# Kernel tuning notes

Hardware: AMD Instinct MI355X
Metric: run time of the kernel (lower is better)

Reference implementation:

```python
import jax, jax.numpy as jnp
import numpy as np

B, I, J, DIN, DOUT = 256, 1152, 10, 8, 16
ROUTING_ITERS = 3


def squash(v):
    # v: [..., D]; squash(v) = (|v|^2 / (1+|v|^2)) * v/|v| = v * |v| / (1+|v|^2)
    l2 = jnp.linalg.norm(v, axis=-1, keepdims=True)
    return v * (l2 / (1.0 + l2 * l2))


def setup_inputs() -> dict:
    key = jax.random.key(0)
    k1, k2 = jax.random.split(key)
    x = jax.random.normal(k1, (B, I, DIN), dtype=jnp.float32)
    # per-(i,j) Linear(DIN -> DOUT, bias=False) weights, stacked: [I, J, DOUT, DIN]
    W = jax.random.normal(k2, (I, J, DOUT, DIN), dtype=jnp.float32) * 0.1
    return {"x": x, "W": W}


def reference(x, W):
    # prediction vectors u[b,i,j,:] = W[i,j] @ x[b,i,:]  -> [B, I, J, DOUT]
    u = jnp.einsum('bid,ijod->bijo', x, W)
    b = jnp.zeros((I, J), dtype=u.dtype)  # routing logits (shared across batch)
    s = None
    for _ in range(ROUTING_ITERS):
        c = jax.nn.softmax(b, axis=-1)              # [I, J]
        s = jnp.einsum('ij,bijd->bjd', c, u)        # coupling-weighted sum over in-caps
        s = squash(s)                               # [B, J, DOUT]
        # agreement: b[i,j] += sum_b <u[b,i,j], s[b,j]>
        b = b + jnp.einsum('bijd,bjd->ij', u, s)
    return s
```

## Files before the change

### kernel.cpp

```cpp
#include <hip/hip_runtime.h>
#include <math.h>

typedef unsigned short ushort_t;
typedef __attribute__((ext_vector_type(8))) __bf16 bf16x8;
typedef __attribute__((ext_vector_type(4))) float floatx4;

#define B_    256
#define I_    1152
#define J_    10
#define DIN_  8
#define DOUT_ 16
#define K_    (I_*DIN_)
#define N_    (J_*DOUT_)
#define KSPLIT 16
#define KCHUNK (K_/KSPLIT)
#define KSTEPS (KCHUNK/32)

#define CHUNK16 2368

static __device__ __forceinline__ ushort_t f2bf(float f) {
    unsigned int u = __float_as_uint(f);
    u += 0x7fffu + ((u >> 16) & 1u);
    return (ushort_t)(u >> 16);
}
static __device__ __forceinline__ float bf2f(ushort_t h) {
    return __uint_as_float(((unsigned int)h) << 16);
}

__global__ __launch_bounds__(256)
void prep_xpack_kernel(const float* __restrict__ x, ushort_t* __restrict__ xPk)
{
    const int gid = blockIdx.x * 256 + threadIdx.x;
    const int f   = gid * 8;
    const int row = f / K_;
    const int kk  = f - row * K_;
    const int kc  = kk / KCHUNK;
    const int t   = kk - kc * KCHUNK;
    const int s   = t >> 5;
    const int q   = (t & 31) >> 3;
    const int mb  = row >> 4, r = row & 15;

    const float* src = x + (size_t)f;
    bf16x8 h8, l8;
    #pragma unroll
    for (int e = 0; e < 8; ++e) {
        float v = src[e];
        __bf16 h = (__bf16)v;
        h8[e] = h;
        l8[e] = (__bf16)(v - (float)h);
    }
    bf16x8* dst = (bf16x8*)xPk + (size_t)(mb * 16 + kc) * CHUNK16 + s * 128 + q * 16 + r;
    dst[0]  = h8;
    dst[64] = l8;
}

__global__ __launch_bounds__(256)
void prep_wpack_kernel(const float* __restrict__ W, float* __restrict__ wPk)
{
    const int gid = blockIdx.x * 256 + threadIdx.x;
    const int f   = gid * 4;
    const int i   = f / 1280;
    const int rem = f - i * 1280;
    const int no  = rem >> 3;
    const int p   = (rem >> 2) & 1;
    const int nt  = no >> 4, r = no & 15;
    const int kc  = i / 72;
    const int m   = i - kc * 72;
    const int s   = m >> 2, q = m & 3;

    float4 v = *(const float4*)(W + (size_t)f);
    ((float4*)wPk)[(size_t)(nt * 16 + kc) * CHUNK16 + (s * 2 + p) * 64 + q * 16 + r] = v;
}

__global__ __launch_bounds__(128)
void gemm_s_part_kernel(const ushort_t* __restrict__ xPk, const float* __restrict__ wPk,
                        const float* __restrict__ blog,
                        float* __restrict__ pbuf, const int iter)
{
    const int tid  = threadIdx.x;
    const int blk  = blockIdx.x;
    const int kb   = blk & 7;
    const int tile = blk >> 3;
    const int mb   = tile & 15;
    const int nt   = tile >> 4;
    const int lane = tid & 63;
    const int w    = tid >> 6;
    const int kc   = kb * 2 + w;

    __shared__ float   c_lds[144];
    __shared__ floatx4 part[2 * 64];

    if (iter > 0) {
        for (int r2 = tid; r2 < 144; r2 += 128) {
            const float* br = blog + (size_t)(kb * 144 + r2) * J_;
            float bv[J_];
            float mx = -1e30f;
            #pragma unroll
            for (int j = 0; j < J_; ++j) { bv[j] = br[j]; mx = fmaxf(mx, bv[j]); }
            float sum = 0.f;
            #pragma unroll
            for (int j = 0; j < J_; ++j) { bv[j] = __expf(bv[j] - mx); sum += bv[j]; }
            c_lds[r2] = bv[nt] / sum;
        }
        __syncthreads();
    }

    {
        const int q = lane >> 4;
        const bf16x8* xp = (const bf16x8*)xPk + (size_t)(mb * 16 + kc) * CHUNK16 + lane;
        const float4* wp = (const float4*)wPk + (size_t)(nt * 16 + kc) * CHUNK16 + lane;
        floatx4 acc = {0.f, 0.f, 0.f, 0.f};

        bf16x8 rah[2], ral[2];
        float4 rw0[2], rw1[2];
        #pragma unroll
        for (int s = 0; s < 2; ++s) {
            rah[s] = xp[s * 128];
            ral[s] = xp[s * 128 + 64];
            rw0[s] = wp[s * 128];
            rw1[s] = wp[s * 128 + 64];
        }
        #pragma unroll
        for (int s = 0; s < KSTEPS; ++s) {
            bf16x8 ah = rah[s & 1], al = ral[s & 1];
            float4 w0 = rw0[s & 1], w1 = rw1[s & 1];
            if (s + 2 < KSTEPS) {
                rah[s & 1] = xp[(s + 2) * 128];
                ral[s & 1] = xp[(s + 2) * 128 + 64];
                rw0[s & 1] = wp[(s + 2) * 128];
                rw1[s & 1] = wp[(s + 2) * 128 + 64];
            }
            float cs = (iter == 0) ? 0.1f : c_lds[w * 72 + 4 * s + q];
            float wvv[8] = {w0.x, w0.y, w0.z, w0.w, w1.x, w1.y, w1.z, w1.w};
            bf16x8 bh, bl;
            #pragma unroll
            for (int e = 0; e < 8; ++e) {
                float pe = wvv[e] * cs;
                __bf16 g = (__bf16)pe;
                bh[e] = g;
                bl[e] = (__bf16)(pe - (float)g);
            }
            acc = __builtin_amdgcn_mfma_f32_16x16x32_bf16(ah, bh, acc, 0, 0, 0);
            acc = __builtin_amdgcn_mfma_f32_16x16x32_bf16(al, bh, acc, 0, 0, 0);
            acc = __builtin_amdgcn_mfma_f32_16x16x32_bf16(ah, bl, acc, 0, 0, 0);
        }
        part[w * 64 + lane] = acc;
    }
    __syncthreads();

    const int row  = tid >> 3;
    const int col2 = (tid & 7) * 2;
    float2 v2;
    #pragma unroll
    for (int h = 0; h < 2; ++h) {
        const int o      = col2 + h;
        const int lane_c = ((row >> 2) << 4) | o;
        const int reg    = row & 3;
        ((float*)&v2)[h] = part[lane_c][reg] + part[64 + lane_c][reg];
    }
    *(float2*)(pbuf + (size_t)blk * 256 + row * 16 + col2) = v2;
}

__global__ __launch_bounds__(256)
void reduce_squash_kernel(const float* __restrict__ pbuf, float* __restrict__ s_out,
                          ushort_t* __restrict__ Sbt_hi, ushort_t* __restrict__ Sbt_lo,
                          const int iter)
{
    const int tile = blockIdx.x;
    const int mb   = tile & 15;
    const int nt   = tile >> 4;
    const int t    = threadIdx.x;
    const int row  = t >> 4;
    const int o    = t & 15;

    const float* pb = pbuf + (size_t)tile * 8 * 256 + row * 16 + o;
    float v = 0.f;
    #pragma unroll
    for (int u = 0; u < 8; ++u)
        v += pb[u * 256];

    float sq = v * v;
    #pragma unroll
    for (int off = 1; off < 16; off <<= 1)
        sq += __shfl_xor(sq, off, 16);
    float l2 = sqrtf(sq);
    float val = v * (l2 / (1.f + sq));
    const int b  = mb * 16 + row;
    const int jo = nt * 16 + o;
    if (iter == 2) {
        s_out[(size_t)b * N_ + jo] = val;
    } else {
        ushort_t hi = f2bf(val);
        Sbt_hi[(size_t)jo * B_ + b] = hi;
        Sbt_lo[(size_t)jo * B_ + b] = f2bf(val - bf2f(hi));
    }
}

__global__ __launch_bounds__(256)
void gemm_bupd_kernel(const float* __restrict__ x,
                      const ushort_t* __restrict__ Sbt_hi, const ushort_t* __restrict__ Sbt_lo,
                      const float* __restrict__ W, float* __restrict__ blog,
                      const int first)
{
    int wv   = (blockIdx.x & 7) * 360 + (blockIdx.x >> 3) * 4 + (threadIdx.x >> 6);
    int lane = threadIdx.x & 63;
    int mt = wv / 5;
    int jp = wv - mt * 5;
    int j0 = jp * 2, j1 = jp * 2 + 1;
    int r = lane & 15, q = lane >> 4;
    const float* xp = x + (size_t)(8 * q) * K_ + (mt * 16 + r);
    size_t b0off = (size_t)(j0 * 16 + r) * B_ + 8 * q;
    size_t b1off = (size_t)(j1 * 16 + r) * B_ + 8 * q;
    floatx4 acc0 = {0.f, 0.f, 0.f, 0.f};
    floatx4 acc1 = {0.f, 0.f, 0.f, 0.f};

    float xcur[8], xnxt[8];
    #pragma unroll
    for (int e = 0; e < 8; ++e) xcur[e] = xp[(size_t)e * K_];
    #pragma unroll
    for (int s = 0; s < B_ / 32; ++s) {
        if (s + 1 < B_ / 32) {
            #pragma unroll
            for (int e = 0; e < 8; ++e)
                xnxt[e] = xp[(size_t)((s + 1) * 32 + e) * K_];
        }
        bf16x8 ah, al;
        #pragma unroll
        for (int e = 0; e < 8; ++e) {
            float v = xcur[e];
            __bf16 h = (__bf16)v;
            ah[e] = h;
            al[e] = (__bf16)(v - (float)h);
        }
        bf16x8 bh0 = *(const bf16x8*)(Sbt_hi + b0off + s * 32);
        bf16x8 bl0 = *(const bf16x8*)(Sbt_lo + b0off + s * 32);
        bf16x8 bh1 = *(const bf16x8*)(Sbt_hi + b1off + s * 32);
        bf16x8 bl1 = *(const bf16x8*)(Sbt_lo + b1off + s * 32);
        acc0 = __builtin_amdgcn_mfma_f32_16x16x32_bf16(ah, bh0, acc0, 0, 0, 0);
        acc0 = __builtin_amdgcn_mfma_f32_16x16x32_bf16(al, bh0, acc0, 0, 0, 0);
        acc0 = __builtin_amdgcn_mfma_f32_16x16x32_bf16(ah, bl0, acc0, 0, 0, 0);
        acc1 = __builtin_amdgcn_mfma_f32_16x16x32_bf16(ah, bh1, acc1, 0, 0, 0);
        acc1 = __builtin_amdgcn_mfma_f32_16x16x32_bf16(al, bh1, acc1, 0, 0, 0);
        acc1 = __builtin_amdgcn_mfma_f32_16x16x32_bf16(ah, bl1, acc1, 0, 0, 0);
        #pragma unroll
        for (int e = 0; e < 8; ++e) xcur[e] = xnxt[e];
    }
    int i  = mt * 2 + (q >> 1);
    int d0 = (q & 1) * 4;
    int o  = lane & 15;
    int iw = mt * 2 + (lane >> 5);
    {
        const float4 w4 = *(const float4*)(W + ((((size_t)i * J_ + j0) * DOUT_ + o) * DIN_ + d0));
        float val = acc0[0] * w4.x + acc0[1] * w4.y + acc0[2] * w4.z + acc0[3] * w4.w;
        #pragma unroll
        for (int off = 1; off < 32; off <<= 1)
            val += __shfl_xor(val, off, 32);
        if ((lane & 31) == 0) {
            float* dst = blog + (size_t)iw * J_ + j0;
            if (first) *dst = val; else *dst += val;
        }
    }
    {
        const float4 w4 = *(const float4*)(W + ((((size_t)i * J_ + j1) * DOUT_ + o) * DIN_ + d0));
        float val = acc1[0] * w4.x + acc1[1] * w4.y + acc1[2] * w4.z + acc1[3] * w4.w;
        #pragma unroll
        for (int off = 1; off < 32; off <<= 1)
            val += __shfl_xor(val, off, 32);
        if ((lane & 31) == 0) {
            float* dst = blog + (size_t)iw * J_ + j1;
            if (first) *dst = val; else *dst += val;
        }
    }
}

extern "C" void kernel_launch(void* const* d_in, const int* in_sizes, int n_in,
                              void* d_out, int out_size, void* d_ws, size_t ws_size,
                              hipStream_t stream)
{
    const float* x = (const float*)d_in[0];
    const float* W = (const float*)d_in[1];
    float* s_out = (float*)d_out;

    char* ws = (char*)d_ws;
    ushort_t* Sbt_hi = (ushort_t*)(ws);
    ushort_t* Sbt_lo = (ushort_t*)(ws + 81920);
    float*    blog   = (float*)   (ws + 163840);
    float*    pbuf   = (float*)   (ws + 262144);
    ushort_t* xPk    = (ushort_t*)(ws + 1572864);
    float*    wPk    = (float*)   (ws + 11272192);

    prep_xpack_kernel<<<1152, 256, 0, stream>>>(x, xPk);
    prep_wpack_kernel<<<1440, 256, 0, stream>>>(W, wPk);

    for (int it = 0; it < 3; ++it) {
        gemm_s_part_kernel<<<1280, 128, 0, stream>>>(xPk, wPk, blog, pbuf, it);
        reduce_squash_kernel<<<160, 256, 0, stream>>>(pbuf, s_out,
                                                      Sbt_hi, Sbt_lo, it);
        if (it < 2)
            gemm_bupd_kernel<<<720, 256, 0, stream>>>(x, Sbt_hi, Sbt_lo,
                                                      W, blog, it == 0 ? 1 : 0);
    }
}
```

Measured before the change: 135.9 us.

## Register-block gemm_s_part into 2x2 output tiles per block with deeper prefetch

Each block now computes a 2x2 group of (batch-tile, output-tile) products, so each loaded x fragment is reused across two W tiles and each W fragment across two x tiles. Global loads per MFMA drop and the softmax coefficient computation is shared across both output tiles. The prefetch depth rises from 2 to 3 stages. In exchange the grid shrinks from 1280 to 320 blocks, fewer than a few per CU on this GPU, and register pressure rises, which may cut occupancy and latency hiding.

Result: slower. 140.2 us (+3.1%).

```diff
diff --git a/kernel.cpp b/kernel.cpp
--- a/kernel.cpp
+++ b/kernel.cpp
@@ -80,15 +80,17 @@
     const int tid  = threadIdx.x;
     const int blk  = blockIdx.x;
     const int kb   = blk & 7;
-    const int tile = blk >> 3;
-    const int mb   = tile & 15;
-    const int nt   = tile >> 4;
+    const int grp  = blk >> 3;
+    const int mbp  = grp / 5;
+    const int ntp  = grp - mbp * 5;
+    const int mb0  = mbp * 2, mb1 = mbp * 2 + 1;
+    const int nt0  = ntp,     nt1 = ntp + 5;
     const int lane = tid & 63;
     const int w    = tid >> 6;
     const int kc   = kb * 2 + w;
 
-    __shared__ float   c_lds[144];
-    __shared__ floatx4 part[2 * 64];
+    __shared__ float   c2_lds[144 * 2];
+    __shared__ floatx4 part[8 * 64];
 
     if (iter > 0) {
         for (int r2 = tid; r2 < 144; r2 += 128) {
@@ -100,65 +102,98 @@
             float sum = 0.f;
             #pragma unroll
             for (int j = 0; j < J_; ++j) { bv[j] = __expf(bv[j] - mx); sum += bv[j]; }
-            c_lds[r2] = bv[nt] / sum;
+            c2_lds[r2 * 2]     = bv[nt0] / sum;
+            c2_lds[r2 * 2 + 1] = bv[nt1] / sum;
         }
         __syncthreads();
     }
 
     {
         const int q = lane >> 4;
-        const bf16x8* xp = (const bf16x8*)xPk + (size_t)(mb * 16 + kc) * CHUNK16 + lane;
-        const float4* wp = (const float4*)wPk + (size_t)(nt * 16 + kc) * CHUNK16 + lane;
-        floatx4 acc = {0.f, 0.f, 0.f, 0.f};
-
-        bf16x8 rah[2], ral[2];
-        float4 rw0[2], rw1[2];
-        #pragma unroll
-        for (int s = 0; s < 2; ++s) {
-            rah[s] = xp[s * 128];
-            ral[s] = xp[s * 128 + 64];
-            rw0[s] = wp[s * 128];
-            rw1[s] = wp[s * 128 + 64];
+        const bf16x8* xp0 = (const bf16x8*)xPk + (size_t)(mb0 * 16 + kc) * CHUNK16 + lane;
+        const bf16x8* xp1 = (const bf16x8*)xPk + (size_t)(mb1 * 16 + kc) * CHUNK16 + lane;
+        const float4* wq0 = (const float4*)wPk + (size_t)(nt0 * 16 + kc) * CHUNK16 + lane;
+        const float4* wq1 = (const float4*)wPk + (size_t)(nt1 * 16 + kc) * CHUNK16 + lane;
+        floatx4 a00 = {0.f,0.f,0.f,0.f}, a10 = a00, a01 = a00, a11 = a00;
+
+        bf16x8 rh0[3], rl0[3], rh1[3], rl1[3];
+        float4 rw00[3], rw01[3], rw10[3], rw11[3];
+        #pragma unroll
+        for (int s = 0; s < 3; ++s) {
+            rh0[s]  = xp0[s * 128];  rl0[s]  = xp0[s * 128 + 64];
+            rh1[s]  = xp1[s * 128];  rl1[s]  = xp1[s * 128 + 64];
+            rw00[s] = wq0[s * 128];  rw01[s] = wq0[s * 128 + 64];
+            rw10[s] = wq1[s * 128];  rw11[s] = wq1[s * 128 + 64];
         }
         #pragma unroll
         for (int s = 0; s < KSTEPS; ++s) {
-            bf16x8 ah = rah[s & 1], al = ral[s & 1];
-            float4 w0 = rw0[s & 1], w1 = rw1[s & 1];
-            if (s + 2 < KSTEPS) {
-                rah[s & 1] = xp[(s + 2) * 128];
-                ral[s & 1] = xp[(s + 2) * 128 + 64];
-                rw0[s & 1] = wp[(s + 2) * 128];
-                rw1[s & 1] = wp[(s + 2) * 128 + 64];
+            const int sl = s % 3;
+            bf16x8 ah0 = rh0[sl], al0 = rl0[sl], ah1 = rh1[sl], al1 = rl1[sl];
+            float4 w00 = rw00[sl], w01 = rw01[sl], w10 = rw10[sl], w11 = rw11[sl];
+            if (s + 3 < KSTEPS) {
+                rh0[sl]  = xp0[(s + 3) * 128];  rl0[sl]  = xp0[(s + 3) * 128 + 64];
+                rh1[sl]  = xp1[(s + 3) * 128];  rl1[sl]  = xp1[(s + 3) * 128 + 64];
+                rw00[sl] = wq0[(s + 3) * 128];  rw01[sl] = wq0[(s + 3) * 128 + 64];
+                rw10[sl] = wq1[(s + 3) * 128];  rw11[sl] = wq1[(s + 3) * 128 + 64];
             }
-            float cs = (iter == 0) ? 0.1f : c_lds[w * 72 + 4 * s + q];
-            float wvv[8] = {w0.x, w0.y, w0.z, w0.w, w1.x, w1.y, w1.z, w1.w};
-            bf16x8 bh, bl;
+            float cs0, cs1;
+            if (iter == 0) { cs0 = 0.1f; cs1 = 0.1f; }
+            else {
+                const int ii = (w * 72 + 4 * s + q) * 2;
+                cs0 = c2_lds[ii];
+                cs1 = c2_lds[ii + 1];
+            }
+            float wv0[8] = {w00.x, w00.y, w00.z, w00.w, w01.x, w01.y, w01.z, w01.w};
+            float wv1[8] = {w10.x, w10.y, w10.z, w10.w, w11.x, w11.y, w11.z, w11.w};
+            bf16x8 bh0, bl0, bh1, bl1;
             #pragma unroll
             for (int e = 0; e < 8; ++e) {
-                float pe = wvv[e] * cs;
-                __bf16 g = (__bf16)pe;
-                bh[e] = g;
-                bl[e] = (__bf16)(pe - (float)g);
+                float p0 = wv0[e] * cs0;
+                __bf16 g0 = (__bf16)p0;
+                bh0[e] = g0;
+                bl0[e] = (__bf16)(p0 - (float)g0);
+                float p1 = wv1[e] * cs1;
+                __bf16 g1 = (__bf16)p1;
+                bh1[e] = g1;
+                bl1[e] = (__bf16)(p1 - (float)g1);
             }
-            acc = __builtin_amdgcn_mfma_f32_16x16x32_bf16(ah, bh, acc, 0, 0, 0);
-            acc = __builtin_amdgcn_mfma_f32_16x16x32_bf16(al, bh, acc, 0, 0, 0);
-            acc = __builtin_amdgcn_mfma_f32_16x16x32_bf16(ah, bl, acc, 0, 0, 0);
-        }
-        part[w * 64 + lane] = acc;
+            a00 = __builtin_amdgcn_mfma_f32_16x16x32_bf16(ah0, bh0, a00, 0, 0, 0);
+            a00 = __builtin_amdgcn_mfma_f32_16x16x32_bf16(al0, bh0, a00, 0, 0, 0);
+            a00 = __builtin_amdgcn_mfma_f32_16x16x32_bf16(ah0, bl0, a00, 0, 0, 0);
+            a10 = __builtin_amdgcn_mfma_f32_16x16x32_bf16(ah1, bh0, a10, 0, 0, 0);
+            a10 = __builtin_amdgcn_mfma_f32_16x16x32_bf16(al1, bh0, a10, 0, 0, 0);
+            a10 = __builtin_amdgcn_mfma_f32_16x16x32_bf16(ah1, bl0, a10, 0, 0, 0);
+            a01 = __builtin_amdgcn_mfma_f32_16x16x32_bf16(ah0, bh1, a01, 0, 0, 0);
+            a01 = __builtin_amdgcn_mfma_f32_16x16x32_bf16(al0, bh1, a01, 0, 0, 0);
+            a01 = __builtin_amdgcn_mfma_f32_16x16x32_bf16(ah0, bl1, a01, 0, 0, 0);
+            a11 = __builtin_amdgcn_mfma_f32_16x16x32_bf16(ah1, bh1, a11, 0, 0, 0);
+            a11 = __builtin_amdgcn_mfma_f32_16x16x32_bf16(al1, bh1, a11, 0, 0, 0);
+            a11 = __builtin_amdgcn_mfma_f32_16x16x32_bf16(ah1, bl1, a11, 0, 0, 0);
+        }
+        part[(w * 4 + 0) * 64 + lane] = a00;
+        part[(w * 4 + 1) * 64 + lane] = a10;
+        part[(w * 4 + 2) * 64 + lane] = a01;
+        part[(w * 4 + 3) * 64 + lane] = a11;
     }
     __syncthreads();
 
     const int row  = tid >> 3;
     const int col2 = (tid & 7) * 2;
-    float2 v2;
-    #pragma unroll
-    for (int h = 0; h < 2; ++h) {
-        const int o      = col2 + h;
-        const int lane_c = ((row >> 2) << 4) | o;
-        const int reg    = row & 3;
-        ((float*)&v2)[h] = part[lane_c][reg] + part[64 + lane_c][reg];
-    }
-    *(float2*)(pbuf + (size_t)blk * 256 + row * 16 + col2) = v2;
+    #pragma unroll
+    for (int t4 = 0; t4 < 4; ++t4) {
+        const int mb = (t4 & 1) ? mb1 : mb0;
+        const int nt = (t4 >> 1) ? nt1 : nt0;
+        float2 v2;
+        #pragma unroll
+        for (int h = 0; h < 2; ++h) {
+            const int o      = col2 + h;
+            const int lane_c = ((row >> 2) << 4) | o;
+            const int reg    = row & 3;
+            ((float*)&v2)[h] = part[(0 * 4 + t4) * 64 + lane_c][reg]
+                             + part[(1 * 4 + t4) * 64 + lane_c][reg];
+        }
+        *(float2*)(pbuf + ((size_t)(nt * 16 + mb) * 8 + kb) * 256 + row * 16 + col2) = v2;
+    }
 }
 
 __global__ __launch_bounds__(256)
@@ -293,7 +328,7 @@
     prep_wpack_kernel<<<1440, 256, 0, stream>>>(W, wPk);
 
     for (int it = 0; it < 3; ++it) {
-        gemm_s_part_kernel<<<1280, 128, 0, stream>>>(xPk, wPk, blog, pbuf, it);
+        gemm_s_part_kernel<<<320, 128, 0, stream>>>(xPk, wPk, blog, pbuf, it);
         reduce_squash_kernel<<<160, 256, 0, stream>>>(pbuf, s_out,
                                                       Sbt_hi, Sbt_lo, it);
         if (it < 2)
```

## Merge prep kernels and split GEMM K-steps across four waves per block

Applied to the files above, without the earlier changes.

The two packing kernels are fused into one launch that picks its x or W path from the block index, which removes one kernel launch. The partial-S GEMM now runs 256 threads per block. Each pair of waves splits the 18 K-steps of a chunk into two halves of 9, so each wave runs a shorter serial MFMA chain and more waves are resident to hide latency. The cost is a four-way LDS reduction of the partials and more LDS per block.

Measured after the change: 135.5 us, median of 3. Within noise of the previous version (-0.3%).

```diff
diff --git a/kernel.cpp b/kernel.cpp
--- a/kernel.cpp
+++ b/kernel.cpp
@@ -15,7 +15,6 @@
 #define KSPLIT 16
 #define KCHUNK (K_/KSPLIT)
 #define KSTEPS (KCHUNK/32)
-
 #define CHUNK16 2368
 
 static __device__ __forceinline__ ushort_t f2bf(float f) {
@@ -28,70 +27,72 @@
 }
 
 __global__ __launch_bounds__(256)
-void prep_xpack_kernel(const float* __restrict__ x, ushort_t* __restrict__ xPk)
-{
-    const int gid = blockIdx.x * 256 + threadIdx.x;
-    const int f   = gid * 8;
-    const int row = f / K_;
-    const int kk  = f - row * K_;
-    const int kc  = kk / KCHUNK;
-    const int t   = kk - kc * KCHUNK;
-    const int s   = t >> 5;
-    const int q   = (t & 31) >> 3;
-    const int mb  = row >> 4, r = row & 15;
-
-    const float* src = x + (size_t)f;
-    bf16x8 h8, l8;
-    #pragma unroll
-    for (int e = 0; e < 8; ++e) {
-        float v = src[e];
-        __bf16 h = (__bf16)v;
-        h8[e] = h;
-        l8[e] = (__bf16)(v - (float)h);
-    }
-    bf16x8* dst = (bf16x8*)xPk + (size_t)(mb * 16 + kc) * CHUNK16 + s * 128 + q * 16 + r;
-    dst[0]  = h8;
-    dst[64] = l8;
+void prep_all_kernel(const float* __restrict__ x, const float* __restrict__ W,
+                     ushort_t* __restrict__ xPk, float* __restrict__ wPk)
+{
+    const int blk = blockIdx.x;
+    const int tid = threadIdx.x;
+
+    if (blk < 1152) {
+        const int gid = blk * 256 + tid;
+        const int f   = gid * 8;
+        const int row = f / K_;
+        const int kk  = f - row * K_;
+        const int kc  = kk / KCHUNK;
+        const int t   = kk - kc * KCHUNK;
+        const int s   = t >> 5;
+        const int q   = (t & 31) >> 3;
+        const int mb  = row >> 4, r = row & 15;
+
+        const float* src = x + (size_t)f;
+        bf16x8 h8, l8;
+        #pragma unroll
+        for (int e = 0; e < 8; ++e) {
+            float v = src[e];
+            __bf16 h = (__bf16)v;
+            h8[e] = h;
+            l8[e] = (__bf16)(v - (float)h);
+        }
+        bf16x8* dst = (bf16x8*)xPk + (size_t)(mb * 16 + kc) * CHUNK16 + s * 128 + q * 16 + r;
+        dst[0]  = h8;
+        dst[64] = l8;
+    } else {
+        const int gid = (blk - 1152) * 256 + tid;
+        const int f   = gid * 4;
+        const int i   = f / 1280;
+        const int rem = f - i * 1280;
+        const int no  = rem >> 3;
+        const int p   = (rem >> 2) & 1;
+        const int nt  = no >> 4, r = no & 15;
+        const int kc  = i / 72;
+        const int m   = i - kc * 72;
+        const int s   = m >> 2, q = m & 3;
+        float4 v = *(const float4*)(W + (size_t)f);
+        ((float4*)wPk)[(size_t)(nt * 16 + kc) * CHUNK16 + (s * 2 + p) * 64 + q * 16 + r] = v;
+    }
 }
 
 __global__ __launch_bounds__(256)
-void prep_wpack_kernel(const float* __restrict__ W, float* __restrict__ wPk)
-{
-    const int gid = blockIdx.x * 256 + threadIdx.x;
-    const int f   = gid * 4;
-    const int i   = f / 1280;
-    const int rem = f - i * 1280;
-    const int no  = rem >> 3;
-    const int p   = (rem >> 2) & 1;
-    const int nt  = no >> 4, r = no & 15;
-    const int kc  = i / 72;
-    const int m   = i - kc * 72;
-    const int s   = m >> 2, q = m & 3;
-
-    float4 v = *(const float4*)(W + (size_t)f);
-    ((float4*)wPk)[(size_t)(nt * 16 + kc) * CHUNK16 + (s * 2 + p) * 64 + q * 16 + r] = v;
-}
-
-__global__ __launch_bounds__(128)
 void gemm_s_part_kernel(const ushort_t* __restrict__ xPk, const float* __restrict__ wPk,
                         const float* __restrict__ blog,
                         float* __restrict__ pbuf, const int iter)
 {
-    const int tid  = threadIdx.x;
-    const int blk  = blockIdx.x;
-    const int kb   = blk & 7;
-    const int tile = blk >> 3;
-    const int mb   = tile & 15;
-    const int nt   = tile >> 4;
-    const int lane = tid & 63;
-    const int w    = tid >> 6;
-    const int kc   = kb * 2 + w;
+    const int tid   = threadIdx.x;
+    const int blk   = blockIdx.x;
+    const int kb    = blk & 7;
+    const int tile  = blk >> 3;
+    const int mb    = tile & 15;
+    const int nt    = tile >> 4;
+    const int lane  = tid & 63;
+    const int w     = tid >> 6;
+    const int kc    = kb * 2 + (w >> 1);
+    const int shalf = w & 1;
 
     __shared__ float   c_lds[144];
-    __shared__ floatx4 part[2 * 64];
+    __shared__ floatx4 part[4 * 64];
 
     if (iter > 0) {
-        for (int r2 = tid; r2 < 144; r2 += 128) {
+        for (int r2 = tid; r2 < 144; r2 += 256) {
             const float* br = blog + (size_t)(kb * 144 + r2) * J_;
             float bv[J_];
             float mx = -1e30f;
@@ -107,8 +108,11 @@
 
     {
         const int q = lane >> 4;
-        const bf16x8* xp = (const bf16x8*)xPk + (size_t)(mb * 16 + kc) * CHUNK16 + lane;
-        const float4* wp = (const float4*)wPk + (size_t)(nt * 16 + kc) * CHUNK16 + lane;
+        const int sbase = shalf * 9;
+        const bf16x8* xp = (const bf16x8*)xPk + (size_t)(mb * 16 + kc) * CHUNK16
+                           + sbase * 128 + lane;
+        const float4* wp = (const float4*)wPk + (size_t)(nt * 16 + kc) * CHUNK16
+                           + sbase * 128 + lane;
         floatx4 acc = {0.f, 0.f, 0.f, 0.f};
 
         bf16x8 rah[2], ral[2];
@@ -121,16 +125,17 @@
             rw1[s] = wp[s * 128 + 64];
         }
         #pragma unroll
-        for (int s = 0; s < KSTEPS; ++s) {
+        for (int s = 0; s < 9; ++s) {
             bf16x8 ah = rah[s & 1], al = ral[s & 1];
             float4 w0 = rw0[s & 1], w1 = rw1[s & 1];
-            if (s + 2 < KSTEPS) {
+            if (s + 2 < 9) {
                 rah[s & 1] = xp[(s + 2) * 128];
                 ral[s & 1] = xp[(s + 2) * 128 + 64];
                 rw0[s & 1] = wp[(s + 2) * 128];
                 rw1[s & 1] = wp[(s + 2) * 128 + 64];
             }
-            float cs = (iter == 0) ? 0.1f : c_lds[w * 72 + 4 * s + q];
+            float cs = (iter == 0) ? 0.1f
+                                   : c_lds[(w >> 1) * 72 + 4 * (sbase + s) + q];
             float wvv[8] = {w0.x, w0.y, w0.z, w0.w, w1.x, w1.y, w1.z, w1.w};
             bf16x8 bh, bl;
             #pragma unroll
@@ -148,17 +153,13 @@
     }
     __syncthreads();
 
-    const int row  = tid >> 3;
-    const int col2 = (tid & 7) * 2;
-    float2 v2;
-    #pragma unroll
-    for (int h = 0; h < 2; ++h) {
-        const int o      = col2 + h;
-        const int lane_c = ((row >> 2) << 4) | o;
-        const int reg    = row & 3;
-        ((float*)&v2)[h] = part[lane_c][reg] + part[64 + lane_c][reg];
-    }
-    *(float2*)(pbuf + (size_t)blk * 256 + row * 16 + col2) = v2;
+    const int row = tid >> 4;
+    const int o   = tid & 15;
+    const int lane_c = ((row >> 2) << 4) | o;
+    const int reg    = row & 3;
+    float v = part[0 * 64 + lane_c][reg] + part[1 * 64 + lane_c][reg]
+            + part[2 * 64 + lane_c][reg] + part[3 * 64 + lane_c][reg];
+    pbuf[(size_t)blk * 256 + row * 16 + o] = v;
 }
 
 __global__ __launch_bounds__(256)
@@ -289,11 +290,10 @@
     ushort_t* xPk    = (ushort_t*)(ws + 1572864);
     float*    wPk    = (float*)   (ws + 11272192);
 
-    prep_xpack_kernel<<<1152, 256, 0, stream>>>(x, xPk);
-    prep_wpack_kernel<<<1440, 256, 0, stream>>>(W, wPk);
+    prep_all_kernel<<<2592, 256, 0, stream>>>(x, W, xPk, wPk);
 
     for (int it = 0; it < 3; ++it) {
-        gemm_s_part_kernel<<<1280, 128, 0, stream>>>(xPk, wPk, blog, pbuf, it);
+        gemm_s_part_kernel<<<1280, 256, 0, stream>>>(xPk, wPk, blog, pbuf, it);
         reduce_squash_kernel<<<160, 256, 0, stream>>>(pbuf, s_out,
                                                       Sbt_hi, Sbt_lo, it);
         if (it < 2)
```
